# Kernel tuning notes

Hardware: AMD Instinct MI355X
Metric: run time of the kernel (lower is better)

Reference implementation:

```python
import jax, jax.numpy as jnp
import numpy as np

K = 8                      # neighbors per node (module default)
MUL0, MUL1, MUL2 = 64, 32, 16   # multiplicities of 0e, 1o, 2e
D = MUL0 + 3 * MUL1 + 5 * MUL2  # 240 = irreps dim


def _w3j_112():
    """Wigner-3j-like coupling 1 x 1 -> 2 (real basis), Frobenius norm 1 like e3nn."""
    M = np.zeros((5, 3, 3), dtype=np.float32)
    s = 1.0 / np.sqrt(2.0)
    M[0, 0, 1] = M[0, 1, 0] = s          # xy
    M[1, 0, 2] = M[1, 2, 0] = s          # xz
    M[2, 1, 2] = M[2, 2, 1] = s          # yz
    M[3, 0, 0] = s; M[3, 1, 1] = -s      # x^2 - y^2
    t = 1.0 / np.sqrt(6.0)
    M[4, 0, 0] = -t; M[4, 1, 1] = -t; M[4, 2, 2] = 2 * t  # 2z^2 - x^2 - y^2
    return jnp.asarray(np.transpose(M, (1, 2, 0)) / np.sqrt(5.0))  # [3,3,5]

C112 = _w3j_112()                         # coupling for 1o x 1o -> 2e
C211 = jnp.transpose(C112, (2, 0, 1))     # cyclic permutation: 2e x 1o -> 1o


def _knn_edges(coords, k):
    """Per-batch kNN graph; returns flat (senders, receivers) into [B*N] node ids."""
    B, N, _ = coords.shape
    d2 = jnp.sum((coords[:, :, None, :] - coords[:, None, :, :]) ** 2, -1)  # [B,N,N]
    d2 = d2 + jnp.eye(N, dtype=coords.dtype) * 1e9  # exclude self
    _, nbr = jax.lax.top_k(-d2, k)                  # [B,N,k] neighbor indices
    offs = (jnp.arange(B) * N)[:, None, None]
    senders = (nbr + offs).reshape(-1)
    receivers = jnp.broadcast_to(jnp.arange(N)[None, :, None] + offs, (B, N, k)).reshape(-1)
    return senders, receivers


def setup_inputs() -> dict:
    key = jax.random.key(0)
    ks = jax.random.split(key, 9)
    B, N = 4, 4096
    return {
        "node_feats": jax.random.normal(ks[0], (B, N, D), jnp.float32),
        "coords": jax.random.normal(ks[1], (B, N, 3), jnp.float32) * 10.0,
        "W1": jax.random.normal(ks[2], (MUL0, MUL1), jnp.float32),  # 0e x 1o -> 1o
        "W2": jax.random.normal(ks[3], (MUL1, MUL0), jnp.float32),  # 1o x 1o -> 0e
        "W3": jax.random.normal(ks[4], (MUL1, MUL2), jnp.float32),  # 1o x 1o -> 2e
        "W4": jax.random.normal(ks[5], (MUL2, MUL1), jnp.float32),  # 2e x 1o -> 1o
        "L0": jax.random.normal(ks[6], (MUL0, MUL0), jnp.float32),
        "L1": jax.random.normal(ks[7], (MUL1, MUL1), jnp.float32),
        "L2": jax.random.normal(ks[8], (MUL2, MUL2), jnp.float32),
    }


def reference(node_feats, coords, W1, W2, W3, W4, L0, L1, L2):
    B, N, _ = node_feats.shape
    senders, receivers = _knn_edges(coords, K)
    cf = coords.reshape(-1, 3)
    ev = cf[senders] - cf[receivers]              # [E,3] edge vectors (1x1o)
    xj = node_feats.reshape(-1, D)[senders]       # per-edge gather of sender feats
    x0 = xj[:, :MUL0]                             # [E,64]   0e
    x1 = xj[:, MUL0:MUL0 + 3 * MUL1].reshape(-1, MUL1, 3)  # [E,32,3] 1o
    x2 = xj[:, MUL0 + 3 * MUL1:].reshape(-1, MUL2, 5)      # [E,16,5] 2e

    # FullyConnectedTensorProduct (component irrep norm, 'element' path norm)
    # fan_in to 1o output: MUL0 + MUL2 = 80; to 0e: 32; to 2e: 32.
    m1 = jnp.sqrt(1.0 / (MUL0 + MUL2)) * jnp.einsum('eu,ek,uw->ewk', x0, ev, W1)
    m1 = m1 + jnp.sqrt(3.0 / (MUL0 + MUL2)) * jnp.einsum('eua,ajk,ej,uw->ewk', x2, C211, ev, W4)
    m0 = jnp.sqrt(1.0 / (3.0 * MUL1)) * jnp.einsum('eui,ei,uw->ew', x1, ev, W2)
    m2 = jnp.sqrt(5.0 / MUL1) * jnp.einsum('eui,ej,ijk,uw->ewk', x1, ev, C112, W3)
    msg = jnp.concatenate([m0, m1.reshape(-1, 3 * MUL1), m2.reshape(-1, 5 * MUL2)], axis=-1)

    # scatter-add aggregation at receivers
    agg = jax.ops.segment_sum(msg, receivers, num_segments=B * N)  # [B*N, D]

    # equivariant Linear: per-irrep multiplicity mixing, fan_in-normalized
    y0 = (agg[:, :MUL0] @ L0) / jnp.sqrt(float(MUL0))
    y1 = jnp.einsum('nuk,uw->nwk', agg[:, MUL0:MUL0 + 3 * MUL1].reshape(-1, MUL1, 3), L1) / jnp.sqrt(float(MUL1))
    y2 = jnp.einsum('nuk,uw->nwk', agg[:, MUL0 + 3 * MUL1:].reshape(-1, MUL2, 5), L2) / jnp.sqrt(float(MUL2))
    out = jnp.concatenate([y0, y1.reshape(-1, 3 * MUL1), y2.reshape(-1, 5 * MUL2)], axis=-1)
    return out.reshape(B, N, D)
```

## Files before the change

kernel.cpp:

```cpp
#include <hip/hip_runtime.h>

#define NN   4096
#define KNBR 8
#define DF   240
#define NSUB 16
#define QPB  64

__device__ __forceinline__ void insD(float v, float t[KNBR]) {
#pragma unroll
  for (int k = KNBR - 1; k >= 1; k--)
    t[k] = __builtin_amdgcn_fmed3f(t[k - 1], t[k], v);
  t[0] = fminf(t[0], v);
}

__device__ __forceinline__ void insertDI(float d2, int j, float bd[KNBR],
                                         int bi[KNBR]) {
#pragma unroll
  for (int k = KNBR - 1; k >= 1; k--) {
    bool mk  = d2 < bd[k];
    bool mk1 = d2 < bd[k - 1];
    bd[k] = mk ? (mk1 ? bd[k - 1] : d2) : bd[k];
    bi[k] = mk ? (mk1 ? bi[k - 1] : j) : bi[k];
  }
  bool m0 = d2 < bd[0];
  bd[0] = m0 ? d2 : bd[0];
  bi[0] = m0 ? j : bi[0];
}

__global__ __launch_bounds__(1024, 4) void knn_all(
    const float* __restrict__ coords,
    const float* __restrict__ W1, const float* __restrict__ W2,
    const float* __restrict__ W3, const float* __restrict__ W4,
    const float* __restrict__ L0, const float* __restrict__ L1,
    const float* __restrict__ L2, float* __restrict__ Wf,
    int* __restrict__ nbr) {
  if (blockIdx.x >= 256) {
    const float sA = 0.012757759076995719f;
    const float sB = 0.019764235376052370f;
    const float sC = 0.034232659844072875f;
    const float sD = 0.098821176880261850f;
    int idx = (blockIdx.x - 256) * 1024 + threadIdx.x;
    if (idx < 2048) {
      int u = idx >> 6, c = idx & 63;
      float a = 0.f;
#pragma unroll 8
      for (int m = 0; m < 64; m++) a += W2[u * 64 + m] * L0[m * 64 + c];
      Wf[idx] = sA * a;
    } else if (idx < 4096) {
      int t = idx - 2048;
      int u = t >> 5, c = t & 31;
      float a = 0.f;
#pragma unroll 8
      for (int m = 0; m < 32; m++) a += W1[u * 32 + m] * L1[m * 32 + c];
      Wf[idx] = sB * a;
    } else if (idx < 4608) {
      int t = idx - 4096;
      int u = t >> 5, c = t & 31;
      float a = 0.f;
#pragma unroll 8
      for (int m = 0; m < 32; m++) a += W4[u * 32 + m] * L1[m * 32 + c];
      Wf[idx] = sC * a;
    } else {
      int t = idx - 4608;
      int u = t >> 4, c = t & 15;
      float a = 0.f;
#pragma unroll 8
      for (int m = 0; m < 16; m++) a += W3[u * 16 + m] * L2[m * 16 + c];
      Wf[idx] = sD * a;
    }
    return;
  }

  __shared__ float4 cnd[3072];
  __shared__ float pd[NSUB][QPB][KNBR + 1];
  __shared__ unsigned short pi[NSUB][QPB][KNBR + 1];
  __shared__ float thrS[QPB];

  const int blk = blockIdx.x;
  const int b = blk >> 6;
  const int chunk = blk & 63;
  const int qi  = threadIdx.x & 63;
  const int sub = threadIdx.x >> 6;
  const int iq  = chunk * 64 + qi;
  const float* cb = coords + (size_t)b * NN * 3;
  const float4* cb4 = (const float4*)cb;

  {
    int t = threadIdx.x;
    cnd[t]        = cb4[t];
    cnd[1024 + t] = cb4[1024 + t];
    cnd[2048 + t] = cb4[2048 + t];
  }
  const float qx = cb[iq * 3 + 0], qy = cb[iq * 3 + 1], qz = cb[iq * 3 + 2];
  __syncthreads();

  const int j0 = sub * 256;

  float t0v = 3.0e38f, t1v = 3.0e38f;
#pragma unroll 4
  for (int g = 0; g < 64; ++g) {
    int base = j0 + 4 * g;
    int f = 3 * (sub * 64 + g);
    float4 f0 = cnd[f + 0];
    float4 f1 = cnd[f + 1];
    float4 f2 = cnd[f + 2];
    float xs[4] = {f0.x, f0.w, f1.z, f2.y};
    float ys[4] = {f0.y, f1.x, f1.w, f2.z};
    float zs[4] = {f0.z, f1.y, f2.x, f2.w};
#pragma unroll
    for (int c = 0; c < 4; ++c) {
      float dx = xs[c] - qx, dy = ys[c] - qy, dz = zs[c] - qz;
      float d2 = dx * dx + dy * dy + dz * dz;
      d2 = (base + c == iq) ? 3.0e38f : d2;
      t1v = __builtin_amdgcn_fmed3f(t0v, t1v, d2);
      t0v = fminf(t0v, d2);
    }
  }
  pd[sub][qi][0] = t0v;
  pd[sub][qi][1] = t1v;
  __syncthreads();

  if (threadIdx.x < 64) {
    const int q = threadIdx.x;
    float md[KNBR];
#pragma unroll
    for (int k = 0; k < KNBR; k++) md[k] = 3.0e38f;
    for (int s = 0; s < NSUB; s++) {
      insD(pd[s][q][0], md);
      insD(pd[s][q][1], md);
    }
    thrS[q] = md[KNBR - 1];
  }
  __syncthreads();

  const float tq = thrS[qi];
  float bd[KNBR];
  int bi[KNBR];
#pragma unroll
  for (int k = 0; k < KNBR; k++) { bd[k] = 3.0e38f; bi[k] = 0; }
#pragma unroll 2
  for (int g = 0; g < 64; ++g) {
    int base = j0 + 4 * g;
    int f = 3 * (sub * 64 + g);
    float4 f0 = cnd[f + 0];
    float4 f1 = cnd[f + 1];
    float4 f2 = cnd[f + 2];
    float xs[4] = {f0.x, f0.w, f1.z, f2.y};
    float ys[4] = {f0.y, f1.x, f1.w, f2.z};
    float zs[4] = {f0.z, f1.y, f2.x, f2.w};
    float d2s[4];
#pragma unroll
    for (int c = 0; c < 4; ++c) {
      float dx = xs[c] - qx, dy = ys[c] - qy, dz = zs[c] - qz;
      float d2 = dx * dx + dy * dy + dz * dz;
      d2s[c] = (base + c == iq) ? 3.0e38f : d2;
    }
    float m4 = fminf(fminf(d2s[0], d2s[1]), fminf(d2s[2], d2s[3]));
    if (m4 <= tq) {
#pragma unroll
      for (int c = 0; c < 4; ++c)
        if (d2s[c] <= tq) insertDI(d2s[c], base + c, bd, bi);
    }
  }
#pragma unroll
  for (int k = 0; k < KNBR; k++) {
    pd[sub][qi][k] = bd[k];
    pi[sub][qi][k] = (unsigned short)bi[k];
  }
  __syncthreads();

  if (threadIdx.x < 64) {
    const int q = threadIdx.x;
    float md[KNBR];
    int mi[KNBR];
#pragma unroll
    for (int k = 0; k < KNBR; k++) { md[k] = 3.0e38f; mi[k] = 0; }
    for (int s = 0; s < NSUB; s++) {
#pragma unroll
      for (int k = 0; k < KNBR; k++) {
        float vd = pd[s][q][k];
        if (vd < md[KNBR - 1]) insertDI(vd, (int)pi[s][q][k], md, mi);
      }
    }
    int* nr = nbr + (size_t)(b * NN + chunk * 64 + q) * KNBR;
#pragma unroll
    for (int k = 0; k < KNBR; k++) nr[k] = b * NN + mi[k];
  }
}

__global__ __launch_bounds__(256, 4) void msg_kernel(
    const float* __restrict__ feats, const float* __restrict__ coords,
    const int* __restrict__ nbr, const float* __restrict__ Wf,
    float* __restrict__ out) {
  __shared__ float accb[4][432];
  __shared__ float sev[4][KNBR][3];
  __shared__ int snb[4][KNBR];

  const int bid = ((blockIdx.x & 7) << 9) | (blockIdx.x >> 3);
  const int w = threadIdx.x >> 6;
  const int u = threadIdx.x & 63;
  const int node = bid * 4 + w;

  if (u < KNBR) {
    int jg = nbr[(size_t)node * KNBR + u];
    snb[w][u] = jg;
    sev[w][u][0] = coords[(size_t)jg * 3 + 0] - coords[(size_t)node * 3 + 0];
    sev[w][u][1] = coords[(size_t)jg * 3 + 1] - coords[(size_t)node * 3 + 1];
    sev[w][u][2] = coords[(size_t)jg * 3 + 2] - coords[(size_t)node * 3 + 2];
  }
  __syncthreads();

  const float S_ = 0.31622776601683794f;
  const float T_ = 0.18257418583505536f;

  float z0x = 0.f, z0y = 0.f, z0z = 0.f;
  float s1 = 0.f, p0 = 0.f, p1 = 0.f, p2 = 0.f, p3 = 0.f, p4 = 0.f;
  float q0 = 0.f, q1 = 0.f, q2 = 0.f;

#pragma unroll
  for (int h = 0; h < 2; h++) {
    const float* fr[4];
    float xv[4], av0[4], av1[4], av2[4];
    float bv0[4], bv1[4], bv2[4], bv3[4], bv4[4];
#pragma unroll
    for (int i = 0; i < 4; i++) {
      fr[i] = feats + (size_t)snb[w][4 * h + i] * DF;
      xv[i] = fr[i][u];
    }
    if (u < 32) {
#pragma unroll
      for (int i = 0; i < 4; i++) {
        av0[i] = fr[i][64 + 3 * u];
        av1[i] = fr[i][65 + 3 * u];
        av2[i] = fr[i][66 + 3 * u];
      }
      if (u < 16) {
#pragma unroll
        for (int i = 0; i < 4; i++) {
          bv0[i] = fr[i][160 + 5 * u];
          bv1[i] = fr[i][161 + 5 * u];
          bv2[i] = fr[i][162 + 5 * u];
          bv3[i] = fr[i][163 + 5 * u];
          bv4[i] = fr[i][164 + 5 * u];
        }
      }
    }
#pragma unroll
    for (int i = 0; i < 4; i++) {
      const int e = 4 * h + i;
      float X = sev[w][e][0], Y = sev[w][e][1], Z = sev[w][e][2];
      float sxv = S_ * X, syv = S_ * Y, szv = S_ * Z;
      float txv = T_ * X, tyv = T_ * Y, t2z = 2.f * T_ * Z;
      z0x += xv[i] * X;
      z0y += xv[i] * Y;
      z0z += xv[i] * Z;
      if (u < 32) {
        s1 += av0[i] * X + av1[i] * Y + av2[i] * Z;
        p0 += av0[i] * syv + av1[i] * sxv;
        p1 += av0[i] * szv + av2[i] * sxv;
        p2 += av1[i] * szv + av2[i] * syv;
        p3 += av0[i] * sxv - av1[i] * syv;
        p4 += av2[i] * t2z - av0[i] * txv - av1[i] * tyv;
        if (u < 16) {
          q0 += bv0[i] * syv + bv1[i] * szv + bv3[i] * sxv - bv4[i] * txv;
          q1 += bv0[i] * sxv + bv2[i] * szv - bv3[i] * syv - bv4[i] * tyv;
          q2 += bv1[i] * sxv + bv2[i] * syv + bv4[i] * t2z;
        }
      }
    }
  }

  float* A = accb[w];
  A[32 + 3 * u + 0] = z0x;
  A[32 + 3 * u + 1] = z0y;
  A[32 + 3 * u + 2] = z0z;
  if (u < 32) {
    A[u] = s1;
    float* pp = A + 224 + 5 * u;
    pp[0] = p0; pp[1] = p1; pp[2] = p2; pp[3] = p3; pp[4] = p4;
  }
  if (u < 16) {
    float* qq = A + 384 + 3 * u;
    qq[0] = q0; qq[1] = q1; qq[2] = q2;
  }
  __syncthreads();

  const float* WA = Wf;
  const float* WB = Wf + 2048;
  const float* WC = Wf + 4096;
  const float* WD = Wf + 4608;
  float* orow = out + (size_t)node * DF;

  {
    float a = 0.f;
#pragma unroll
    for (int m = 0; m < 32; m++) a += A[m] * WA[m * 64 + u];
    orow[u] = a;
  }
#pragma unroll
  for (int m0 = 0; m0 < 96; m0 += 64) {
    int m = m0 + u;
    if (m < 96) {
      int w1 = m / 3, k = m - w1 * 3;
      float a = 0.f;
#pragma unroll
      for (int t = 0; t < 64; t++) a += A[32 + 3 * t + k] * WB[t * 32 + w1];
#pragma unroll
      for (int t = 0; t < 16; t++) a += A[384 + 3 * t + k] * WC[t * 32 + w1];
      orow[64 + m] = a;
    }
  }
#pragma unroll
  for (int m0 = 0; m0 < 80; m0 += 64) {
    int m = m0 + u;
    if (m < 80) {
      int w2 = m / 5, k = m - w2 * 5;
      float a = 0.f;
#pragma unroll
      for (int t = 0; t < 32; t++) a += A[224 + 5 * t + k] * WD[t * 16 + w2];
      orow[160 + m] = a;
    }
  }
}

extern "C" void kernel_launch(void* const* d_in, const int* in_sizes, int n_in,
                              void* d_out, int out_size, void* d_ws,
                              size_t ws_size, hipStream_t stream) {
  const float* feats  = (const float*)d_in[0];
  const float* coords = (const float*)d_in[1];
  const float* W1 = (const float*)d_in[2];
  const float* W2 = (const float*)d_in[3];
  const float* W3 = (const float*)d_in[4];
  const float* W4 = (const float*)d_in[5];
  const float* L0 = (const float*)d_in[6];
  const float* L1 = (const float*)d_in[7];
  const float* L2 = (const float*)d_in[8];
  float* out = (float*)d_out;

  float* Wf  = (float*)d_ws;
  int*   nbr = (int*)((float*)d_ws + 5120);

  knn_all<<<261, 1024, 0, stream>>>(coords, W1, W2, W3, W4, L0, L1, L2, Wf,
                                    nbr);
  msg_kernel<<<4096, 256, 0, stream>>>(feats, coords, nbr, Wf, out);
}
```

Before: 190.2 us.

## Fuse kNN search, weight folding and message aggregation into one kernel

Merges the kNN kernel and the message/linear kernel into a single launch of 256 blocks of 1024 threads. Each block keeps its neighbor lists, edge vectors and folded weights in a shared LDS buffer, recomputing the folded weights per block. Each wave then processes four nodes in turn, and only a per-wave waitcnt orders the accumulator writes before they are read. The first pass drops its per-candidate self check by taking the 9th smallest distance as the threshold. This removes a launch, the global neighbor/weight round trip and the second kernel's index loads. The cost is lower occupancy during the bandwidth-bound gather phase and redundant weight folding in every block.

Result: no change. 190.2 us (-0.0%).

```diff
diff --git a/kernel.cpp b/kernel.cpp
--- a/kernel.cpp
+++ b/kernel.cpp
@@ -6,9 +6,19 @@
 #define NSUB 16
 #define QPB  64
 
-__device__ __forceinline__ void insD(float v, float t[KNBR]) {
-#pragma unroll
-  for (int k = KNBR - 1; k >= 1; k--)
+#define OFF_PD   49152
+#define OFF_PI   86016
+#define OFF_THR  104448
+#define OFF_NBR  104704
+#define OFF_WF   0
+#define OFF_SEV  20480
+#define OFF_SNB  26624
+#define OFF_ACC  28672
+#define SMEM_SZ  106752
+
+__device__ __forceinline__ void insD9(float v, float t[9]) {
+#pragma unroll
+  for (int k = 8; k >= 1; k--)
     t[k] = __builtin_amdgcn_fmed3f(t[k - 1], t[k], v);
   t[0] = fminf(t[0], v);
 }
@@ -27,54 +37,13 @@
   bi[0] = m0 ? j : bi[0];
 }
 
-__global__ __launch_bounds__(1024, 4) void knn_all(
-    const float* __restrict__ coords,
+__global__ __launch_bounds__(1024, 4) void fused_all(
+    const float* __restrict__ feats, const float* __restrict__ coords,
     const float* __restrict__ W1, const float* __restrict__ W2,
     const float* __restrict__ W3, const float* __restrict__ W4,
     const float* __restrict__ L0, const float* __restrict__ L1,
-    const float* __restrict__ L2, float* __restrict__ Wf,
-    int* __restrict__ nbr) {
-  if (blockIdx.x >= 256) {
-    const float sA = 0.012757759076995719f;
-    const float sB = 0.019764235376052370f;
-    const float sC = 0.034232659844072875f;
-    const float sD = 0.098821176880261850f;
-    int idx = (blockIdx.x - 256) * 1024 + threadIdx.x;
-    if (idx < 2048) {
-      int u = idx >> 6, c = idx & 63;
-      float a = 0.f;
-#pragma unroll 8
-      for (int m = 0; m < 64; m++) a += W2[u * 64 + m] * L0[m * 64 + c];
-      Wf[idx] = sA * a;
-    } else if (idx < 4096) {
-      int t = idx - 2048;
-      int u = t >> 5, c = t & 31;
-      float a = 0.f;
-#pragma unroll 8
-      for (int m = 0; m < 32; m++) a += W1[u * 32 + m] * L1[m * 32 + c];
-      Wf[idx] = sB * a;
-    } else if (idx < 4608) {
-      int t = idx - 4096;
-      int u = t >> 5, c = t & 31;
-      float a = 0.f;
-#pragma unroll 8
-      for (int m = 0; m < 32; m++) a += W4[u * 32 + m] * L1[m * 32 + c];
-      Wf[idx] = sC * a;
-    } else {
-      int t = idx - 4608;
-      int u = t >> 4, c = t & 15;
-      float a = 0.f;
-#pragma unroll 8
-      for (int m = 0; m < 16; m++) a += W3[u * 16 + m] * L2[m * 16 + c];
-      Wf[idx] = sD * a;
-    }
-    return;
-  }
-
-  __shared__ float4 cnd[3072];
-  __shared__ float pd[NSUB][QPB][KNBR + 1];
-  __shared__ unsigned short pi[NSUB][QPB][KNBR + 1];
-  __shared__ float thrS[QPB];
+    const float* __restrict__ L2, float* __restrict__ out) {
+  __shared__ __align__(16) char smem[SMEM_SZ];
 
   const int blk = blockIdx.x;
   const int b = blk >> 6;
@@ -85,6 +54,12 @@
   const float* cb = coords + (size_t)b * NN * 3;
   const float4* cb4 = (const float4*)cb;
 
+  float4* cnd = (float4*)smem;
+  float* pdB = (float*)(smem + OFF_PD);
+  unsigned short* piB = (unsigned short*)(smem + OFF_PI);
+  float* thrS = (float*)(smem + OFF_THR);
+  int* nbrL = (int*)(smem + OFF_NBR);
+
   {
     int t = threadIdx.x;
     cnd[t]        = cb4[t];
@@ -99,7 +74,6 @@
   float t0v = 3.0e38f, t1v = 3.0e38f;
 #pragma unroll 4
   for (int g = 0; g < 64; ++g) {
-    int base = j0 + 4 * g;
     int f = 3 * (sub * 64 + g);
     float4 f0 = cnd[f + 0];
     float4 f1 = cnd[f + 1];
@@ -111,25 +85,24 @@
     for (int c = 0; c < 4; ++c) {
       float dx = xs[c] - qx, dy = ys[c] - qy, dz = zs[c] - qz;
       float d2 = dx * dx + dy * dy + dz * dz;
-      d2 = (base + c == iq) ? 3.0e38f : d2;
       t1v = __builtin_amdgcn_fmed3f(t0v, t1v, d2);
       t0v = fminf(t0v, d2);
     }
   }
-  pd[sub][qi][0] = t0v;
-  pd[sub][qi][1] = t1v;
+  pdB[(sub * 64 + qi) * 9 + 0] = t0v;
+  pdB[(sub * 64 + qi) * 9 + 1] = t1v;
   __syncthreads();
 
   if (threadIdx.x < 64) {
     const int q = threadIdx.x;
-    float md[KNBR];
-#pragma unroll
-    for (int k = 0; k < KNBR; k++) md[k] = 3.0e38f;
+    float md[9];
+#pragma unroll
+    for (int k = 0; k < 9; k++) md[k] = 3.0e38f;
     for (int s = 0; s < NSUB; s++) {
-      insD(pd[s][q][0], md);
-      insD(pd[s][q][1], md);
-    }
-    thrS[q] = md[KNBR - 1];
+      insD9(pdB[(s * 64 + q) * 9 + 0], md);
+      insD9(pdB[(s * 64 + q) * 9 + 1], md);
+    }
+    thrS[q] = md[8];
   }
   __syncthreads();
 
@@ -164,8 +137,8 @@
   }
 #pragma unroll
   for (int k = 0; k < KNBR; k++) {
-    pd[sub][qi][k] = bd[k];
-    pi[sub][qi][k] = (unsigned short)bi[k];
+    pdB[(sub * 64 + qi) * 9 + k] = bd[k];
+    piB[(sub * 64 + qi) * 9 + k] = (unsigned short)bi[k];
   }
   __syncthreads();
 
@@ -178,148 +151,191 @@
     for (int s = 0; s < NSUB; s++) {
 #pragma unroll
       for (int k = 0; k < KNBR; k++) {
-        float vd = pd[s][q][k];
-        if (vd < md[KNBR - 1]) insertDI(vd, (int)pi[s][q][k], md, mi);
-      }
-    }
-    int* nr = nbr + (size_t)(b * NN + chunk * 64 + q) * KNBR;
-#pragma unroll
-    for (int k = 0; k < KNBR; k++) nr[k] = b * NN + mi[k];
-  }
-}
-
-__global__ __launch_bounds__(256, 4) void msg_kernel(
-    const float* __restrict__ feats, const float* __restrict__ coords,
-    const int* __restrict__ nbr, const float* __restrict__ Wf,
-    float* __restrict__ out) {
-  __shared__ float accb[4][432];
-  __shared__ float sev[4][KNBR][3];
-  __shared__ int snb[4][KNBR];
-
-  const int bid = ((blockIdx.x & 7) << 9) | (blockIdx.x >> 3);
+        float vd = pdB[(s * 64 + q) * 9 + k];
+        if (vd < md[KNBR - 1]) insertDI(vd, (int)piB[(s * 64 + q) * 9 + k],
+                                        md, mi);
+      }
+    }
+#pragma unroll
+    for (int k = 0; k < KNBR; k++) nbrL[q * KNBR + k] = mi[k];
+  }
+  __syncthreads();
+
+  float* WfL  = (float*)(smem + OFF_WF);
+  float* sevL = (float*)(smem + OFF_SEV);
+  int*   snbL = (int*)(smem + OFF_SNB);
+  float* accL = (float*)(smem + OFF_ACC);
+
+  {
+    const float sA = 0.012757759076995719f;
+    const float sB = 0.019764235376052370f;
+    const float sC = 0.034232659844072875f;
+    const float sD = 0.098821176880261850f;
+#pragma unroll
+    for (int i = 0; i < 5; i++) {
+      int idx = threadIdx.x + 1024 * i;
+      if (idx < 2048) {
+        int u2 = idx >> 6, c = idx & 63;
+        float a = 0.f;
+#pragma unroll 8
+        for (int m = 0; m < 64; m++) a += W2[u2 * 64 + m] * L0[m * 64 + c];
+        WfL[idx] = sA * a;
+      } else if (idx < 4096) {
+        int t = idx - 2048;
+        int u2 = t >> 5, c = t & 31;
+        float a = 0.f;
+#pragma unroll 8
+        for (int m = 0; m < 32; m++) a += W1[u2 * 32 + m] * L1[m * 32 + c];
+        WfL[idx] = sB * a;
+      } else if (idx < 4608) {
+        int t = idx - 4096;
+        int u2 = t >> 5, c = t & 31;
+        float a = 0.f;
+#pragma unroll 8
+        for (int m = 0; m < 32; m++) a += W4[u2 * 32 + m] * L1[m * 32 + c];
+        WfL[idx] = sC * a;
+      } else {
+        int t = idx - 4608;
+        int u2 = t >> 4, c = t & 15;
+        float a = 0.f;
+#pragma unroll 8
+        for (int m = 0; m < 16; m++) a += W3[u2 * 16 + m] * L2[m * 16 + c];
+        WfL[idx] = sD * a;
+      }
+    }
+  }
+  if (threadIdx.x < 512) {
+    int t = threadIdx.x;
+    int nl = t >> 3, e = t & 7;
+    int jj = nbrL[nl * KNBR + e];
+    int iqn = chunk * 64 + nl;
+    snbL[t] = b * NN + jj;
+    sevL[3 * t + 0] = cb[jj * 3 + 0] - cb[iqn * 3 + 0];
+    sevL[3 * t + 1] = cb[jj * 3 + 1] - cb[iqn * 3 + 1];
+    sevL[3 * t + 2] = cb[jj * 3 + 2] - cb[iqn * 3 + 2];
+  }
+  __syncthreads();
+
+  const float S_ = 0.31622776601683794f;
+  const float T_ = 0.18257418583505536f;
   const int w = threadIdx.x >> 6;
   const int u = threadIdx.x & 63;
-  const int node = bid * 4 + w;
-
-  if (u < KNBR) {
-    int jg = nbr[(size_t)node * KNBR + u];
-    snb[w][u] = jg;
-    sev[w][u][0] = coords[(size_t)jg * 3 + 0] - coords[(size_t)node * 3 + 0];
-    sev[w][u][1] = coords[(size_t)jg * 3 + 1] - coords[(size_t)node * 3 + 1];
-    sev[w][u][2] = coords[(size_t)jg * 3 + 2] - coords[(size_t)node * 3 + 2];
-  }
-  __syncthreads();
-
-  const float S_ = 0.31622776601683794f;
-  const float T_ = 0.18257418583505536f;
-
-  float z0x = 0.f, z0y = 0.f, z0z = 0.f;
-  float s1 = 0.f, p0 = 0.f, p1 = 0.f, p2 = 0.f, p3 = 0.f, p4 = 0.f;
-  float q0 = 0.f, q1 = 0.f, q2 = 0.f;
-
-#pragma unroll
-  for (int h = 0; h < 2; h++) {
-    const float* fr[4];
-    float xv[4], av0[4], av1[4], av2[4];
-    float bv0[4], bv1[4], bv2[4], bv3[4], bv4[4];
-#pragma unroll
-    for (int i = 0; i < 4; i++) {
-      fr[i] = feats + (size_t)snb[w][4 * h + i] * DF;
-      xv[i] = fr[i][u];
-    }
+  float* A = accL + w * 432;
+
+  for (int i2 = 0; i2 < 4; i2++) {
+    const int nl = w * 4 + i2;
+    const int node = blk * 64 + nl;
+
+    float z0x = 0.f, z0y = 0.f, z0z = 0.f;
+    float s1 = 0.f, p0 = 0.f, p1 = 0.f, p2 = 0.f, p3 = 0.f, p4 = 0.f;
+    float q0 = 0.f, q1 = 0.f, q2 = 0.f;
+
+#pragma unroll
+    for (int h = 0; h < 2; h++) {
+      const float* fr[4];
+      float xv[4], av0[4], av1[4], av2[4];
+      float bv0[4], bv1[4], bv2[4], bv3[4], bv4[4];
+#pragma unroll
+      for (int i = 0; i < 4; i++) {
+        fr[i] = feats + (size_t)snbL[nl * KNBR + 4 * h + i] * DF;
+        xv[i] = fr[i][u];
+      }
+      if (u < 32) {
+#pragma unroll
+        for (int i = 0; i < 4; i++) {
+          av0[i] = fr[i][64 + 3 * u];
+          av1[i] = fr[i][65 + 3 * u];
+          av2[i] = fr[i][66 + 3 * u];
+        }
+        if (u < 16) {
+#pragma unroll
+          for (int i = 0; i < 4; i++) {
+            bv0[i] = fr[i][160 + 5 * u];
+            bv1[i] = fr[i][161 + 5 * u];
+            bv2[i] = fr[i][162 + 5 * u];
+            bv3[i] = fr[i][163 + 5 * u];
+            bv4[i] = fr[i][164 + 5 * u];
+          }
+        }
+      }
+#pragma unroll
+      for (int i = 0; i < 4; i++) {
+        const int e = 4 * h + i;
+        float X = sevL[(nl * KNBR + e) * 3 + 0];
+        float Y = sevL[(nl * KNBR + e) * 3 + 1];
+        float Z = sevL[(nl * KNBR + e) * 3 + 2];
+        float sxv = S_ * X, syv = S_ * Y, szv = S_ * Z;
+        float txv = T_ * X, tyv = T_ * Y, t2z = 2.f * T_ * Z;
+        z0x += xv[i] * X;
+        z0y += xv[i] * Y;
+        z0z += xv[i] * Z;
+        if (u < 32) {
+          s1 += av0[i] * X + av1[i] * Y + av2[i] * Z;
+          p0 += av0[i] * syv + av1[i] * sxv;
+          p1 += av0[i] * szv + av2[i] * sxv;
+          p2 += av1[i] * szv + av2[i] * syv;
+          p3 += av0[i] * sxv - av1[i] * syv;
+          p4 += av2[i] * t2z - av0[i] * txv - av1[i] * tyv;
+          if (u < 16) {
+            q0 += bv0[i] * syv + bv1[i] * szv + bv3[i] * sxv - bv4[i] * txv;
+            q1 += bv0[i] * sxv + bv2[i] * szv - bv3[i] * syv - bv4[i] * tyv;
+            q2 += bv1[i] * sxv + bv2[i] * syv + bv4[i] * t2z;
+          }
+        }
+      }
+    }
+
+    A[32 + 3 * u + 0] = z0x;
+    A[32 + 3 * u + 1] = z0y;
+    A[32 + 3 * u + 2] = z0z;
     if (u < 32) {
-#pragma unroll
-      for (int i = 0; i < 4; i++) {
-        av0[i] = fr[i][64 + 3 * u];
-        av1[i] = fr[i][65 + 3 * u];
-        av2[i] = fr[i][66 + 3 * u];
-      }
-      if (u < 16) {
-#pragma unroll
-        for (int i = 0; i < 4; i++) {
-          bv0[i] = fr[i][160 + 5 * u];
-          bv1[i] = fr[i][161 + 5 * u];
-          bv2[i] = fr[i][162 + 5 * u];
-          bv3[i] = fr[i][163 + 5 * u];
-          bv4[i] = fr[i][164 + 5 * u];
-        }
-      }
-    }
-#pragma unroll
-    for (int i = 0; i < 4; i++) {
-      const int e = 4 * h + i;
-      float X = sev[w][e][0], Y = sev[w][e][1], Z = sev[w][e][2];
-      float sxv = S_ * X, syv = S_ * Y, szv = S_ * Z;
-      float txv = T_ * X, tyv = T_ * Y, t2z = 2.f * T_ * Z;
-      z0x += xv[i] * X;
-      z0y += xv[i] * Y;
-      z0z += xv[i] * Z;
-      if (u < 32) {
-        s1 += av0[i] * X + av1[i] * Y + av2[i] * Z;
-        p0 += av0[i] * syv + av1[i] * sxv;
-        p1 += av0[i] * szv + av2[i] * sxv;
-        p2 += av1[i] * szv + av2[i] * syv;
-        p3 += av0[i] * sxv - av1[i] * syv;
-        p4 += av2[i] * t2z - av0[i] * txv - av1[i] * tyv;
-        if (u < 16) {
-          q0 += bv0[i] * syv + bv1[i] * szv + bv3[i] * sxv - bv4[i] * txv;
-          q1 += bv0[i] * sxv + bv2[i] * szv - bv3[i] * syv - bv4[i] * tyv;
-          q2 += bv1[i] * sxv + bv2[i] * syv + bv4[i] * t2z;
-        }
-      }
-    }
-  }
-
-  float* A = accb[w];
-  A[32 + 3 * u + 0] = z0x;
-  A[32 + 3 * u + 1] = z0y;
-  A[32 + 3 * u + 2] = z0z;
-  if (u < 32) {
-    A[u] = s1;
-    float* pp = A + 224 + 5 * u;
-    pp[0] = p0; pp[1] = p1; pp[2] = p2; pp[3] = p3; pp[4] = p4;
-  }
-  if (u < 16) {
-    float* qq = A + 384 + 3 * u;
-    qq[0] = q0; qq[1] = q1; qq[2] = q2;
-  }
-  __syncthreads();
-
-  const float* WA = Wf;
-  const float* WB = Wf + 2048;
-  const float* WC = Wf + 4096;
-  const float* WD = Wf + 4608;
-  float* orow = out + (size_t)node * DF;
-
-  {
-    float a = 0.f;
-#pragma unroll
-    for (int m = 0; m < 32; m++) a += A[m] * WA[m * 64 + u];
-    orow[u] = a;
-  }
-#pragma unroll
-  for (int m0 = 0; m0 < 96; m0 += 64) {
-    int m = m0 + u;
-    if (m < 96) {
-      int w1 = m / 3, k = m - w1 * 3;
+      A[u] = s1;
+      float* pp = A + 224 + 5 * u;
+      pp[0] = p0; pp[1] = p1; pp[2] = p2; pp[3] = p3; pp[4] = p4;
+    }
+    if (u < 16) {
+      float* qq = A + 384 + 3 * u;
+      qq[0] = q0; qq[1] = q1; qq[2] = q2;
+    }
+    asm volatile("s_waitcnt lgkmcnt(0)" ::: "memory");
+
+    const float* WA = WfL;
+    const float* WB = WfL + 2048;
+    const float* WC = WfL + 4096;
+    const float* WD = WfL + 4608;
+    float* orow = out + (size_t)node * DF;
+
+    {
       float a = 0.f;
 #pragma unroll
-      for (int t = 0; t < 64; t++) a += A[32 + 3 * t + k] * WB[t * 32 + w1];
-#pragma unroll
-      for (int t = 0; t < 16; t++) a += A[384 + 3 * t + k] * WC[t * 32 + w1];
-      orow[64 + m] = a;
-    }
-  }
-#pragma unroll
-  for (int m0 = 0; m0 < 80; m0 += 64) {
-    int m = m0 + u;
-    if (m < 80) {
-      int w2 = m / 5, k = m - w2 * 5;
-      float a = 0.f;
-#pragma unroll
-      for (int t = 0; t < 32; t++) a += A[224 + 5 * t + k] * WD[t * 16 + w2];
-      orow[160 + m] = a;
-    }
+      for (int m = 0; m < 32; m++) a += A[m] * WA[m * 64 + u];
+      orow[u] = a;
+    }
+#pragma unroll
+    for (int m0 = 0; m0 < 96; m0 += 64) {
+      int m = m0 + u;
+      if (m < 96) {
+        int w1 = m / 3, k = m - w1 * 3;
+        float a = 0.f;
+#pragma unroll
+        for (int t = 0; t < 64; t++) a += A[32 + 3 * t + k] * WB[t * 32 + w1];
+#pragma unroll
+        for (int t = 0; t < 16; t++) a += A[384 + 3 * t + k] * WC[t * 32 + w1];
+        orow[64 + m] = a;
+      }
+    }
+#pragma unroll
+    for (int m0 = 0; m0 < 80; m0 += 64) {
+      int m = m0 + u;
+      if (m < 80) {
+        int w2 = m / 5, k = m - w2 * 5;
+        float a = 0.f;
+#pragma unroll
+        for (int t = 0; t < 32; t++) a += A[224 + 5 * t + k] * WD[t * 16 + w2];
+        orow[160 + m] = a;
+      }
+    }
+    asm volatile("s_waitcnt lgkmcnt(0)" ::: "memory");
   }
 }
 
@@ -336,11 +352,8 @@
   const float* L1 = (const float*)d_in[7];
   const float* L2 = (const float*)d_in[8];
   float* out = (float*)d_out;
-
-  float* Wf  = (float*)d_ws;
-  int*   nbr = (int*)((float*)d_ws + 5120);
-
-  knn_all<<<261, 1024, 0, stream>>>(coords, W1, W2, W3, W4, L0, L1, L2, Wf,
-                                    nbr);
-  msg_kernel<<<4096, 256, 0, stream>>>(feats, coords, nbr, Wf, out);
+  (void)d_ws; (void)ws_size;
+
+  fused_all<<<256, 1024, 0, stream>>>(feats, coords, W1, W2, W3, W4, L0, L1,
+                                      L2, out);
 }
```
